# Optimization experiments

Hardware: AMD Instinct MI355X
Metric: run time of the kernel (lower is better)

Reference implementation:

```python
import jax, jax.numpy as jnp
import numpy as np

N_CELLS = 8192
IN_DIM = 512
HID_DIM = 1024
OUT_DIM = 512
ENG_DIM = 128  # hardcoded MLP width in BenchMind
N_FACTIONS = 8
SYNC = 0.15
DEBATE = 0.15


def setup_inputs() -> dict:
    key = jax.random.key(0)
    ks = iter(jax.random.split(key, 40))

    def rn(shape, s=1.0):
        return jax.random.normal(next(ks), shape, dtype=jnp.float32) * s

    def lin(out_d, in_d):
        s = 1.0 / np.sqrt(in_d)
        return rn((out_d, in_d), s), rn((out_d,), s)

    a_W1, a_b1 = lin(ENG_DIM, IN_DIM + HID_DIM)
    a_W2, a_b2 = lin(OUT_DIM, ENG_DIM)
    g_W1, g_b1 = lin(ENG_DIM, IN_DIM + HID_DIM)
    g_W2, g_b2 = lin(OUT_DIM, ENG_DIM)
    gru_Wih, gru_bih = lin(3 * HID_DIM, OUT_DIM + 1)
    gru_Whh, gru_bhh = lin(3 * HID_DIM, HID_DIM)
    proj_W, proj_b = lin(HID_DIM, 2 * HID_DIM)
    head_W, head_b = lin(IN_DIM, OUT_DIM)

    psi = rn((N_CELLS, HID_DIM), 0.1)
    psi = psi / (jnp.linalg.norm(psi, axis=-1, keepdims=True) + 1e-8)
    rho_diag = psi ** 2
    rho_offdiag = rn((N_CELLS, HID_DIM), 0.1)
    hiddens = rn((N_CELLS, HID_DIM), 0.1)
    noise_diag = rn((N_CELLS, HID_DIM))
    noise_off = rn((N_CELLS, HID_DIM))
    x = rn((1, IN_DIM))
    gamma = jnp.float32(0.1)

    return dict(x=x, rho_diag=rho_diag, rho_offdiag=rho_offdiag, hiddens=hiddens,
                gamma=gamma, proj_W=proj_W, proj_b=proj_b,
                a_W1=a_W1, a_b1=a_b1, a_W2=a_W2, a_b2=a_b2,
                g_W1=g_W1, g_b1=g_b1, g_W2=g_W2, g_b2=g_b2,
                gru_Wih=gru_Wih, gru_bih=gru_bih, gru_Whh=gru_Whh, gru_bhh=gru_bhh,
                head_W=head_W, head_b=head_b,
                noise_diag=noise_diag, noise_off=noise_off, step=10)


def _process(x, rho_diag, rho_offdiag, hiddens, gamma, proj_W, proj_b,
             a_W1, a_b1, a_W2, a_b2, g_W1, g_b1, g_W2, g_b2,
             gru_Wih, gru_bih, gru_Whh, gru_bhh, head_W, head_b,
             noise_diag, noise_off, step):
    n = hiddens.shape[0]
    # --- decohere() --- (gamma used via .item() in torch -> non-differentiable)
    g = jax.lax.stop_gradient(jax.nn.sigmoid(gamma))
    rho_off = rho_offdiag * (1.0 - g)
    rho_d = jax.nn.softmax(rho_diag + noise_diag * g * 0.1, axis=-1)
    feat = jnp.concatenate([rho_d, jnp.abs(rho_off)], axis=-1)        # [N, 2H]
    inj = feat @ proj_W.T + proj_b                                     # [N, H]
    h = hiddens + jax.lax.stop_gradient(inj) * 0.1

    # --- batched BenchMind over all cells (torch loops cells one-by-one) ---
    xb = jnp.broadcast_to(x, (n, x.shape[-1]))
    comb = jnp.concatenate([xb, h], axis=-1)                           # [N, I+H]
    a = jax.nn.relu(comb @ a_W1.T + a_b1) @ a_W2.T + a_b2              # [N, O]
    gg = jax.nn.relu(comb @ g_W1.T + g_b1) @ g_W2.T + g_b2             # [N, O]
    out = a - gg
    tension = jnp.mean(out ** 2, axis=-1, keepdims=True)               # [N, 1]

    # GRUCell (torch gate order: r, z, n); inputs are detached in torch
    mem_in = jax.lax.stop_gradient(jnp.concatenate([out, tension], axis=-1))
    gi = mem_in @ gru_Wih.T + gru_bih                                  # [N, 3H]
    gh = h @ gru_Whh.T + gru_bhh                                       # [N, 3H]
    i_r, i_z, i_n = jnp.split(gi, 3, axis=-1)
    h_r, h_z, h_n = jnp.split(gh, 3, axis=-1)
    r = jax.nn.sigmoid(i_r + h_r)
    z = jax.nn.sigmoid(i_z + h_z)
    nn_ = jnp.tanh(i_n + r * h_n)
    new_h = jax.lax.stop_gradient((1.0 - z) * nn_ + z * h)             # .detach() in torch

    # --- faction_sync_debate ---
    nf = min(N_FACTIONS, n // 2)
    fs = n // nf
    hb = new_h[: nf * fs].reshape(nf, fs, -1)
    hb = (1.0 - SYNC) * hb + SYNC * hb.mean(axis=1, keepdims=True)
    if step > 5:
        glob = hb.mean(axis=1).mean(axis=0)                            # [H]
        dc = max(1, fs // 4)
        hb = hb.at[:, :dc].set((1.0 - DEBATE) * hb[:, :dc] + DEBATE * glob)
    new_h = hb.reshape(nf * fs, -1)

    # --- tension-weighted mixture (weights built from .item()s -> no grad) ---
    w = jax.nn.softmax(jax.lax.stop_gradient(tension[:, 0]))           # [N]
    combined = (w[:, None] * out).sum(axis=0, keepdims=True)           # [1, O]
    pred = combined @ head_W.T + head_b                                # [1, I]
    return pred, new_h


def reference(x, rho_diag, rho_offdiag, hiddens, gamma, proj_W, proj_b,
              a_W1, a_b1, a_W2, a_b2, g_W1, g_b1, g_W2, g_b2,
              gru_Wih, gru_bih, gru_Whh, gru_bhh, head_W, head_b,
              noise_diag, noise_off, step):
    return _process(x, rho_diag, rho_offdiag, hiddens, gamma, proj_W, proj_b,
                    a_W1, a_b1, a_W2, a_b2, g_W1, g_b1, g_W2, g_b2,
                    gru_Wih, gru_bih, gru_Whh, gru_bhh, head_W, head_b,
                    noise_diag, noise_off, step)
```

## Files before the change

kernel.cpp:

```cpp
#include <hip/hip_runtime.h>
#include <math.h>

#define NC 8192
#define ID 512
#define HD 1024
#define OD 512
#define ED 128
#define NF 8
#define FS (NC/NF)
#define DC (FS/4)

typedef __bf16 bf16x8 __attribute__((ext_vector_type(8)));
typedef float  f32x4  __attribute__((ext_vector_type(4)));

__device__ __forceinline__ float sigmf(float x){ return 1.0f/(1.0f+__expf(-x)); }

__device__ __forceinline__ unsigned short f2bf(float f){
  union { float f; unsigned u; } v; v.f = f;
  unsigned r = v.u + 0x7FFFu + ((v.u >> 16) & 1u);
  return (unsigned short)(r >> 16);
}
__device__ __forceinline__ float bf2f(unsigned short b){
  union { unsigned u; float f; } v; v.u = ((unsigned)b) << 16;
  return v.f;
}
__device__ __forceinline__ void gload16(const void* g, void* l){
  __builtin_amdgcn_global_load_lds(
      (const __attribute__((address_space(1))) unsigned int*)g,
      (__attribute__((address_space(3))) unsigned int*)l, 16, 0, 0);
}

__global__ __launch_bounds__(256) void k_conv(
    const float* __restrict__ src, unsigned short* __restrict__ dst,
    int rows, int cols, int sld, int sofs, int dld, float scale)
{
  int i = blockIdx.x*256 + threadIdx.x;
  int total = rows*cols/4;
  if (i >= total) return;
  int r = (i*4)/cols, c = (i*4)%cols;
  const float* s = src + (size_t)r*sld + sofs + c;
  unsigned long long pack = 0;
  for (int q=0;q<4;q++)
    pack |= (unsigned long long)f2bf(s[q]*scale) << (16*q);
  *reinterpret_cast<unsigned long long*>(&dst[(size_t)r*dld + c]) = pack;
}

__global__ __launch_bounds__(256) void k_feat(
    const float* __restrict__ rho_diag, const float* __restrict__ noise_diag,
    const float* __restrict__ rho_off,  const float* __restrict__ gamma,
    unsigned short* __restrict__ featb)
{
  int row = blockIdx.x;
  int t = threadIdx.x;
  float g = 1.0f/(1.0f+__expf(-gamma[0]));
  const float* rd = rho_diag  + (size_t)row*HD;
  const float* nd = noise_diag+ (size_t)row*HD;
  const float* ro = rho_off   + (size_t)row*HD;
  unsigned short* f0 = featb + (size_t)row*(2*HD);

  float v[4];
  float mx = -1e30f;
  for (int i=0;i<4;i++){ int j=t+i*256; v[i] = rd[j] + nd[j]*g*0.1f; mx = fmaxf(mx, v[i]); }
  __shared__ float red[256];
  red[t]=mx; __syncthreads();
  for(int s=128;s>0;s>>=1){ if(t<s) red[t]=fmaxf(red[t],red[t+s]); __syncthreads(); }
  mx = red[0]; __syncthreads();
  float sm=0.0f;
  for(int i=0;i<4;i++){ v[i]=__expf(v[i]-mx); sm+=v[i]; }
  red[t]=sm; __syncthreads();
  for(int s=128;s>0;s>>=1){ if(t<s) red[t]+=red[t+s]; __syncthreads(); }
  float inv = 1.0f/red[0];
  float om_g = 1.0f - g;
  for(int i=0;i<4;i++){
    int j=t+i*256;
    f0[j]     = f2bf(v[i]*inv);
    f0[HD+j]  = f2bf(fabsf(ro[j])*om_g);
  }
}

template<int MODE>
__global__ __launch_bounds__(256) void k_mgemm(
    const unsigned short* __restrict__ A,
    const unsigned short* __restrict__ W,
    int K, int N,
    float* __restrict__ Cf, unsigned short* __restrict__ Cb, int ldc,
    const float* __restrict__ e0, const float* __restrict__ e1,
    const float* __restrict__ e2)
{
  __shared__ __attribute__((aligned(16))) unsigned short Asb[128*32];
  __shared__ __attribute__((aligned(16))) unsigned short Bsb[128*32];
  const int t = threadIdx.x;
  const int lane = t & 63, wid = t >> 6;
  const int wr = wid >> 1, wc = wid & 1;
  const int m0 = blockIdx.y * 128, n0 = blockIdx.x * 128;

  const int srow = lane >> 2;
  const int skch = (lane & 3) * 8;
  const int fr = lane & 15, fk = (lane >> 4) * 8;

  f32x4 acc[4][4] = {};
  for (int k0 = 0; k0 < K; k0 += 32) {
    for (int q = 0; q < 2; ++q) {
      int r = wid*32 + q*16 + srow;
      gload16(A + (size_t)(m0 + r)*K + k0 + skch, &Asb[(wid*32 + q*16)*32]);
      gload16(W + (size_t)(n0 + r)*K + k0 + skch, &Bsb[(wid*32 + q*16)*32]);
    }
    __syncthreads();
    bf16x8 af[4], bfr[4];
    for (int i = 0; i < 4; ++i)
      af[i]  = *reinterpret_cast<const bf16x8*>(&Asb[(wr*64 + i*16 + fr)*32 + fk]);
    for (int j = 0; j < 4; ++j)
      bfr[j] = *reinterpret_cast<const bf16x8*>(&Bsb[(wc*64 + j*16 + fr)*32 + fk]);
    for (int i = 0; i < 4; ++i)
      for (int j = 0; j < 4; ++j)
        acc[i][j] = __builtin_amdgcn_mfma_f32_16x16x32_bf16(af[i], bfr[j], acc[i][j], 0, 0, 0);
    __syncthreads();
  }
  const int cr = (lane >> 4) * 4;
  const int cc = lane & 15;
  for (int i = 0; i < 4; ++i){
    for (int j = 0; j < 4; ++j){
      for (int r = 0; r < 4; ++r){
        int m = m0 + wr*64 + i*16 + cr + r;
        int n = n0 + wc*64 + j*16 + cc;
        float v = acc[i][j][r];
        if (MODE == 0)      v = e0[(size_t)m*N + n] + 0.1f*(v + e1[n]);
        else if (MODE == 1) v = fmaxf(v + e0[n], 0.0f);
        else if (MODE == 2) v = v + e0[n];
        else if (MODE == 4) v = v + e0[n] + e1[m]*e2[n];
        size_t o = (size_t)m*ldc + n;
        if (MODE == 0 || MODE == 2) Cf[o] = v;
        Cb[o] = f2bf(v);
      }
    }
  }
}

__global__ __launch_bounds__(128) void k_xpart(
    const float* __restrict__ x,
    const float* __restrict__ aW1, const float* __restrict__ ab1,
    const float* __restrict__ gW1, const float* __restrict__ gb1,
    const float* __restrict__ Wih,
    const float* __restrict__ ab2, const float* __restrict__ gb2,
    float* __restrict__ xcat, float* __restrict__ wlast, float* __restrict__ b2diff)
{
  int t = threadIdx.x;
  if (blockIdx.x == 2){
    for (int n=t; n<3*HD; n+=128) wlast[n] = Wih[(size_t)n*(OD+1) + OD];
    for (int n=t; n<OD;   n+=128) b2diff[n] = ab2[n] - gb2[n];
    return;
  }
  const float* W = blockIdx.x ? gW1 : aW1;
  const float* b = blockIdx.x ? gb1 : ab1;
  float s = b[t];
  const float* wr = W + (size_t)t*(ID+HD);
  for (int k=0;k<ID;k++) s += x[k]*wr[k];
  xcat[blockIdx.x*ED + t] = s;
}

__global__ __launch_bounds__(256) void k_tension(
    const float* __restrict__ outp, float* __restrict__ tens)
{
  int m = blockIdx.x, t = threadIdx.x;
  float s = 0.0f;
  for (int j=t;j<OD;j+=256){ float v = outp[(size_t)m*OD + j]; s += v*v; }
  __shared__ float red[256];
  red[t]=s; __syncthreads();
  for(int k=128;k>0;k>>=1){ if(t<k) red[t]+=red[t+k]; __syncthreads(); }
  if (t==0) tens[m] = red[0] * (1.0f/OD);
}

__global__ __launch_bounds__(256) void k_gru_elem(
    const unsigned short* __restrict__ gi, const unsigned short* __restrict__ gh,
    const float* __restrict__ h, const float* __restrict__ bhh,
    float* __restrict__ newh)
{
  size_t idx = (size_t)blockIdx.x*256 + threadIdx.x;
  int n = (int)(idx & (HD-1));
  size_t m = idx >> 10;
  size_t b = m*(3*HD) + n;
  float i_r = bf2f(gi[b]), i_z = bf2f(gi[b+HD]), i_n = bf2f(gi[b+2*HD]);
  float h_r = bf2f(gh[b]), h_z = bf2f(gh[b+HD]), h_n = bf2f(gh[b+2*HD]);
  float r  = sigmf(i_r + h_r + bhh[n]);
  float z  = sigmf(i_z + h_z + bhh[HD+n]);
  float nn = tanhf(i_n + r*(h_n + bhh[2*HD+n]));
  newh[idx] = (1.0f-z)*nn + z*h[idx];
}

__global__ __launch_bounds__(256) void k_fmean(
    const float* __restrict__ newh, float* __restrict__ fmean)
{
  int f = blockIdx.x;
  int j = blockIdx.y*256 + threadIdx.x;
  const float* base = newh + (size_t)f*FS*HD + j;
  float s = 0.0f;
  for (int c=0;c<FS;c++) s += base[(size_t)c*HD];
  fmean[f*HD + j] = s * (1.0f/FS);
}

__global__ __launch_bounds__(256) void k_sync(
    float* __restrict__ newh, const float* __restrict__ fmean,
    const int* __restrict__ step)
{
  size_t idx = (size_t)blockIdx.x*256 + threadIdx.x;
  int cell = (int)(idx / HD);
  int j    = (int)(idx % HD);
  int f = cell / FS, c = cell % FS;
  float v = newh[idx];
  v = 0.85f*v + 0.15f*fmean[f*HD + j];
  if (step[0] > 5 && c < DC){
    float glob = 0.0f;
    for (int ff=0; ff<NF; ff++) glob += fmean[ff*HD + j];
    glob *= (1.0f/NF);
    v = 0.85f*v + 0.15f*glob;
  }
  newh[idx] = v;
}

__global__ __launch_bounds__(1024) void k_wstats(
    const float* __restrict__ tens, float* __restrict__ stats)
{
  int t = threadIdx.x;
  float mx = -1e30f;
  for (int i=t;i<NC;i+=1024) mx = fmaxf(mx, tens[i]);
  __shared__ float red[1024];
  red[t]=mx; __syncthreads();
  for(int s=512;s>0;s>>=1){ if(t<s) red[t]=fmaxf(red[t],red[t+s]); __syncthreads(); }
  mx = red[0]; __syncthreads();
  float sm=0.0f;
  for (int i=t;i<NC;i+=1024) sm += __expf(tens[i]-mx);
  red[t]=sm; __syncthreads();
  for(int s=512;s>0;s>>=1){ if(t<s) red[t]+=red[t+s]; __syncthreads(); }
  if (t==0){ stats[0]=mx; stats[1]=red[0]; }
}

__global__ __launch_bounds__(256) void k_wnorm(
    const float* __restrict__ tens, const float* __restrict__ stats,
    float* __restrict__ w)
{
  int m = blockIdx.x*256 + threadIdx.x;
  w[m] = __expf(tens[m]-stats[0]) * (1.0f/stats[1]);
}

__global__ __launch_bounds__(256) void k_combined(
    const float* __restrict__ outp, const float* __restrict__ w,
    float* __restrict__ comb)
{
  int n = blockIdx.x, t = threadIdx.x;
  float s = 0.0f;
  for (int m=t; m<NC; m+=256) s += w[m]*outp[(size_t)m*OD + n];
  __shared__ float red[256];
  red[t]=s; __syncthreads();
  for (int sx=128;sx>0;sx>>=1){ if(t<sx) red[t]+=red[t+sx]; __syncthreads(); }
  if (t==0) comb[n] = red[0];
}

__global__ __launch_bounds__(128) void k_pred(
    const float* __restrict__ comb, const float* __restrict__ headW,
    const float* __restrict__ headb, float* __restrict__ pred)
{
  int i = blockIdx.x, t = threadIdx.x;
  float s = 0.0f;
  const float* wr = headW + (size_t)i*OD;
  for (int k=t;k<OD;k+=128) s += comb[k]*wr[k];
  __shared__ float red[128];
  red[t]=s; __syncthreads();
  for (int sx=64;sx>0;sx>>=1){ if(t<sx) red[t]+=red[t+sx]; __syncthreads(); }
  if (t==0) pred[i] = red[0] + headb[i];
}

extern "C" void kernel_launch(void* const* d_in, const int* in_sizes, int n_in,
                              void* d_out, int out_size, void* d_ws, size_t ws_size,
                              hipStream_t stream)
{
  const float* x        = (const float*)d_in[0];
  const float* rho_diag = (const float*)d_in[1];
  const float* rho_off  = (const float*)d_in[2];
  const float* hiddens  = (const float*)d_in[3];
  const float* gamma    = (const float*)d_in[4];
  const float* proj_W   = (const float*)d_in[5];
  const float* proj_b   = (const float*)d_in[6];
  const float* a_W1     = (const float*)d_in[7];
  const float* a_b1     = (const float*)d_in[8];
  const float* a_W2     = (const float*)d_in[9];
  const float* a_b2     = (const float*)d_in[10];
  const float* g_W1     = (const float*)d_in[11];
  const float* g_b1     = (const float*)d_in[12];
  const float* g_W2     = (const float*)d_in[13];
  const float* g_b2     = (const float*)d_in[14];
  const float* gru_Wih  = (const float*)d_in[15];
  const float* gru_bih  = (const float*)d_in[16];
  const float* gru_Whh  = (const float*)d_in[17];
  const float* gru_bhh  = (const float*)d_in[18];
  const float* head_W   = (const float*)d_in[19];
  const float* head_b   = (const float*)d_in[20];
  const float* noise_d  = (const float*)d_in[21];
  const int*   step     = (const int*)d_in[23];

  float* pred = (float*)d_out;
  float* newh = (float*)d_out + ID;

  char* ws = (char*)d_ws;
  const size_t MB = 1024*1024;
  unsigned short* gi_b   = (unsigned short*)(ws + 0);
  unsigned short* featb  = (unsigned short*)(ws + 0);
  unsigned short* gh_b   = (unsigned short*)(ws + 48*MB);
  float*          h_f    = (float*)(ws + 96*MB);
  unsigned short* h_b    = (unsigned short*)(ws + 128*MB);
  float*          outp_f = (float*)(ws + 144*MB);
  unsigned short* outp_b = (unsigned short*)(ws + 160*MB);
  unsigned short* eag    = (unsigned short*)(ws + 168*MB);
  unsigned short* wProj  = (unsigned short*)(ws + 172*MB);
  unsigned short* wWhh   = (unsigned short*)(ws + 176*MB);
  unsigned short* wWih   = (unsigned short*)(ws + 182*MB);
  unsigned short* wEng   = (unsigned short*)(ws + 185*MB);
  unsigned short* wW2    = (unsigned short*)(ws + 185*MB + 512*1024);
  char* sm = ws + 186*MB;
  float* tens   = (float*)(sm + 0);
  float* xcat   = (float*)(sm + 64*1024);
  float* wlast  = (float*)(sm + 128*1024);
  float* b2diff = (float*)(sm + 160*1024);
  float* fmean  = (float*)(sm + 192*1024);
  float* stats  = (float*)(sm + 256*1024);
  float* wts    = (float*)(sm + 320*1024);
  float* comb   = (float*)(sm + 384*1024);

  dim3 blk(256);
  #define CONVGRID(n) dim3(((n)/4 + 255)/256)

  k_conv<<<CONVGRID(1024*2048), blk, 0, stream>>>(proj_W,  wProj, 1024, 2048, 2048, 0, 2048, 1.0f);
  k_conv<<<CONVGRID(3072*1024), blk, 0, stream>>>(gru_Whh, wWhh,  3072, 1024, 1024, 0, 1024, 1.0f);
  k_conv<<<CONVGRID(3072*512),  blk, 0, stream>>>(gru_Wih, wWih,  3072, 512,  513,  0, 512,  1.0f);
  k_conv<<<CONVGRID(128*1024),  blk, 0, stream>>>(a_W1, wEng,            128, 1024, ID+HD, ID, 1024, 1.0f);
  k_conv<<<CONVGRID(128*1024),  blk, 0, stream>>>(g_W1, wEng + 128*1024, 128, 1024, ID+HD, ID, 1024, 1.0f);
  k_conv<<<CONVGRID(512*128),   blk, 0, stream>>>(a_W2, wW2,       512, 128, 128, 0, 256,  1.0f);
  k_conv<<<CONVGRID(512*128),   blk, 0, stream>>>(g_W2, wW2 + 128, 512, 128, 128, 0, 256, -1.0f);

  k_feat<<<dim3(NC), blk, 0, stream>>>(rho_diag, noise_d, rho_off, gamma, featb);
  k_xpart<<<dim3(3), dim3(128), 0, stream>>>(x, a_W1, a_b1, g_W1, g_b1, gru_Wih,
                                             a_b2, g_b2, xcat, wlast, b2diff);

  k_mgemm<0><<<dim3(HD/128, NC/128), blk, 0, stream>>>(
      featb, wProj, 2*HD, HD, h_f, h_b, HD, hiddens, proj_b, nullptr);
  k_mgemm<1><<<dim3(256/128, NC/128), blk, 0, stream>>>(
      h_b, wEng, HD, 256, nullptr, eag, 256, xcat, nullptr, nullptr);
  k_mgemm<2><<<dim3(OD/128, NC/128), blk, 0, stream>>>(
      eag, wW2, 256, OD, outp_f, outp_b, OD, b2diff, nullptr, nullptr);
  k_tension<<<dim3(NC), blk, 0, stream>>>(outp_f, tens);
  k_mgemm<4><<<dim3(3*HD/128, NC/128), blk, 0, stream>>>(
      outp_b, wWih, OD, 3*HD, nullptr, gi_b, 3*HD, gru_bih, tens, wlast);
  k_mgemm<3><<<dim3(3*HD/128, NC/128), blk, 0, stream>>>(
      h_b, wWhh, HD, 3*HD, nullptr, gh_b, 3*HD, nullptr, nullptr, nullptr);
  k_gru_elem<<<dim3((NC*HD)/256), blk, 0, stream>>>(gi_b, gh_b, h_f, gru_bhh, newh);
  k_fmean<<<dim3(NF, HD/256), blk, 0, stream>>>(newh, fmean);
  k_sync<<<dim3((NC*HD)/256), blk, 0, stream>>>(newh, fmean, step);
  k_wstats<<<dim3(1), dim3(1024), 0, stream>>>(tens, stats);
  k_wnorm<<<dim3(NC/256), blk, 0, stream>>>(tens, stats, wts);
  k_combined<<<dim3(OD), blk, 0, stream>>>(outp_f, wts, comb);
  k_pred<<<dim3(ID), dim3(128), 0, stream>>>(comb, head_W, head_b, pred);
}
```

Before: 623.6 us.

## Fuse GRU input and hidden GEMMs with gate epilogue into one kernel

Concatenates the engine output and hidden state into one bf16 activation buffer and packs Wih/Whh into one weight matrix. A single GEMM kernel then computes the r, z and n gate pre-activations in registers and applies the GRU update in its epilogue. This removes the separate gi/gh bf16 intermediates and the elementwise pass. It also adds a grouped block-index swizzle to the GEMMs and splits the weighted-mixture reduction into a two-stage partial sum. The fused kernel uses 64x64 tiles with one wave loading each operand tile, which may lower MFMA efficiency compared with the previous 128x128 tiles.

```diff
diff --git a/kernel.cpp b/kernel.cpp
--- a/kernel.cpp
+++ b/kernel.cpp
@@ -43,6 +43,25 @@
   for (int q=0;q<4;q++)
     pack |= (unsigned long long)f2bf(s[q]*scale) << (16*q);
   *reinterpret_cast<unsigned long long*>(&dst[(size_t)r*dld + c]) = pack;
+}
+
+__global__ __launch_bounds__(256) void k_convgru(
+    const float* __restrict__ Wih, const float* __restrict__ Whh,
+    unsigned short* __restrict__ dst)
+{
+  int i = blockIdx.x*256 + threadIdx.x;
+  const int total = 3*1024*1536/4;
+  if (i >= total) return;
+  int row = (i*4)/1536, c = (i*4)%1536;
+  unsigned long long pack = 0;
+  if (c < 512){
+    const float* s = Wih + (size_t)row*(OD+1) + c;
+    for (int q=0;q<4;q++) pack |= (unsigned long long)f2bf(s[q]) << (16*q);
+  } else {
+    const float* s = Whh + (size_t)row*HD + (c-512);
+    for (int q=0;q<4;q++) pack |= (unsigned long long)f2bf(s[q]) << (16*q);
+  }
+  *reinterpret_cast<unsigned long long*>(&dst[(size_t)row*1536 + c]) = pack;
 }
 
 __global__ __launch_bounds__(256) void k_feat(
@@ -80,19 +99,23 @@
 
 template<int MODE>
 __global__ __launch_bounds__(256) void k_mgemm(
-    const unsigned short* __restrict__ A,
+    const unsigned short* __restrict__ A, int lda,
     const unsigned short* __restrict__ W,
     int K, int N,
-    float* __restrict__ Cf, unsigned short* __restrict__ Cb, int ldc,
-    const float* __restrict__ e0, const float* __restrict__ e1,
-    const float* __restrict__ e2)
+    float* __restrict__ Cf, int ldcf,
+    unsigned short* __restrict__ Cb, int ldcb,
+    const float* __restrict__ e0, const float* __restrict__ e1)
 {
   __shared__ __attribute__((aligned(16))) unsigned short Asb[128*32];
   __shared__ __attribute__((aligned(16))) unsigned short Bsb[128*32];
   const int t = threadIdx.x;
   const int lane = t & 63, wid = t >> 6;
   const int wr = wid >> 1, wc = wid & 1;
-  const int m0 = blockIdx.y * 128, n0 = blockIdx.x * 128;
+
+  const int nwg = gridDim.x*gridDim.y;
+  const int bid = blockIdx.y*gridDim.x + blockIdx.x;
+  const int swz = (bid & 7)*(nwg >> 3) + (bid >> 3);
+  const int m0 = (swz / gridDim.x) * 128, n0 = (swz % gridDim.x) * 128;
 
   const int srow = lane >> 2;
   const int skch = (lane & 3) * 8;
@@ -102,8 +125,8 @@
   for (int k0 = 0; k0 < K; k0 += 32) {
     for (int q = 0; q < 2; ++q) {
       int r = wid*32 + q*16 + srow;
-      gload16(A + (size_t)(m0 + r)*K + k0 + skch, &Asb[(wid*32 + q*16)*32]);
-      gload16(W + (size_t)(n0 + r)*K + k0 + skch, &Bsb[(wid*32 + q*16)*32]);
+      gload16(A + (size_t)(m0 + r)*lda + k0 + skch, &Asb[(wid*32 + q*16)*32]);
+      gload16(W + (size_t)(n0 + r)*K   + k0 + skch, &Bsb[(wid*32 + q*16)*32]);
     }
     __syncthreads();
     bf16x8 af[4], bfr[4];
@@ -127,10 +150,93 @@
         if (MODE == 0)      v = e0[(size_t)m*N + n] + 0.1f*(v + e1[n]);
         else if (MODE == 1) v = fmaxf(v + e0[n], 0.0f);
         else if (MODE == 2) v = v + e0[n];
-        else if (MODE == 4) v = v + e0[n] + e1[m]*e2[n];
-        size_t o = (size_t)m*ldc + n;
-        if (MODE == 0 || MODE == 2) Cf[o] = v;
-        Cb[o] = f2bf(v);
+        if (MODE == 2) Cf[(size_t)m*ldcf + n] = v;
+        Cb[(size_t)m*ldcb + n] = f2bf(v);
+      }
+    }
+  }
+}
+
+__global__ __launch_bounds__(256) void k_gru_mega(
+    const unsigned short* __restrict__ Acat,
+    const unsigned short* __restrict__ Wg,
+    const float* __restrict__ bih, const float* __restrict__ bhh,
+    const float* __restrict__ tens, const float* __restrict__ wlast,
+    float* __restrict__ newh)
+{
+  __shared__ __attribute__((aligned(16))) unsigned short As[64*32];
+  __shared__ __attribute__((aligned(16))) unsigned short Rs[64*32];
+  __shared__ __attribute__((aligned(16))) unsigned short Zs[64*32];
+  __shared__ __attribute__((aligned(16))) unsigned short Ns[64*32];
+  const int t = threadIdx.x;
+  const int lane = t & 63, wid = t >> 6;
+  const int wr = wid >> 1, wc = wid & 1;
+
+  const int nwg = gridDim.x*gridDim.y;
+  const int bid = blockIdx.y*gridDim.x + blockIdx.x;
+  const int swz = (bid & 7)*(nwg >> 3) + (bid >> 3);
+  const int m0 = (swz >> 4) * 64, n0 = (swz & 15) * 64;
+
+  const int srow = lane >> 2;
+  const int skch = (lane & 3) * 8;
+  const int fr = lane & 15, fk = (lane >> 4) * 8;
+
+  const unsigned short* sbase;
+  unsigned short* lbase;
+  if      (wid == 0){ sbase = Acat + (size_t)m0*1536;              lbase = As; }
+  else if (wid == 1){ sbase = Wg   + (size_t)n0*1536;              lbase = Rs; }
+  else if (wid == 2){ sbase = Wg + (size_t)(HD + n0)*1536;         lbase = Zs; }
+  else              { sbase = Wg + (size_t)(2*HD + n0)*1536;       lbase = Ns; }
+
+  f32x4 acc_r[2][2] = {}, acc_z[2][2] = {}, acc_na[2][2] = {}, acc_nb[2][2] = {};
+
+  for (int k0 = 0; k0 < 1536; k0 += 32) {
+    for (int q = 0; q < 4; ++q)
+      gload16(sbase + (size_t)(q*16 + srow)*1536 + k0 + skch, &lbase[(q*16)*32]);
+    __syncthreads();
+    bf16x8 af[2], br[2], bz[2], bn[2];
+    for (int i = 0; i < 2; ++i)
+      af[i] = *reinterpret_cast<const bf16x8*>(&As[(wr*32 + i*16 + fr)*32 + fk]);
+    for (int j = 0; j < 2; ++j){
+      br[j] = *reinterpret_cast<const bf16x8*>(&Rs[(wc*32 + j*16 + fr)*32 + fk]);
+      bz[j] = *reinterpret_cast<const bf16x8*>(&Zs[(wc*32 + j*16 + fr)*32 + fk]);
+      bn[j] = *reinterpret_cast<const bf16x8*>(&Ns[(wc*32 + j*16 + fr)*32 + fk]);
+    }
+    if (k0 < 512){
+      for (int i = 0; i < 2; ++i)
+        for (int j = 0; j < 2; ++j){
+          acc_r [i][j] = __builtin_amdgcn_mfma_f32_16x16x32_bf16(af[i], br[j], acc_r [i][j], 0,0,0);
+          acc_z [i][j] = __builtin_amdgcn_mfma_f32_16x16x32_bf16(af[i], bz[j], acc_z [i][j], 0,0,0);
+          acc_na[i][j] = __builtin_amdgcn_mfma_f32_16x16x32_bf16(af[i], bn[j], acc_na[i][j], 0,0,0);
+        }
+    } else {
+      for (int i = 0; i < 2; ++i)
+        for (int j = 0; j < 2; ++j){
+          acc_r [i][j] = __builtin_amdgcn_mfma_f32_16x16x32_bf16(af[i], br[j], acc_r [i][j], 0,0,0);
+          acc_z [i][j] = __builtin_amdgcn_mfma_f32_16x16x32_bf16(af[i], bz[j], acc_z [i][j], 0,0,0);
+          acc_nb[i][j] = __builtin_amdgcn_mfma_f32_16x16x32_bf16(af[i], bn[j], acc_nb[i][j], 0,0,0);
+        }
+    }
+    __syncthreads();
+  }
+
+  const int cr = (lane >> 4) * 4;
+  const int cc = lane & 15;
+  for (int i = 0; i < 2; ++i){
+    for (int r = 0; r < 4; ++r){
+      int m = m0 + wr*32 + i*16 + cr + r;
+      float tm = tens[m];
+      for (int j = 0; j < 2; ++j){
+        int n = n0 + wc*32 + j*16 + cc;
+        float sr  = acc_r [i][j][r] + bih[n]      + tm*wlast[n]      + bhh[n];
+        float sz  = acc_z [i][j][r] + bih[HD+n]   + tm*wlast[HD+n]   + bhh[HD+n];
+        float sni = acc_na[i][j][r] + bih[2*HD+n] + tm*wlast[2*HD+n];
+        float snh = acc_nb[i][j][r] + bhh[2*HD+n];
+        float rg = sigmf(sr);
+        float zg = sigmf(sz);
+        float nn = tanhf(sni + rg*snh);
+        float hv = bf2f(Acat[(size_t)m*1536 + 512 + n]);
+        newh[(size_t)m*HD + n] = (1.0f - zg)*nn + zg*hv;
       }
     }
   }
@@ -168,23 +274,6 @@
   red[t]=s; __syncthreads();
   for(int k=128;k>0;k>>=1){ if(t<k) red[t]+=red[t+k]; __syncthreads(); }
   if (t==0) tens[m] = red[0] * (1.0f/OD);
-}
-
-__global__ __launch_bounds__(256) void k_gru_elem(
-    const unsigned short* __restrict__ gi, const unsigned short* __restrict__ gh,
-    const float* __restrict__ h, const float* __restrict__ bhh,
-    float* __restrict__ newh)
-{
-  size_t idx = (size_t)blockIdx.x*256 + threadIdx.x;
-  int n = (int)(idx & (HD-1));
-  size_t m = idx >> 10;
-  size_t b = m*(3*HD) + n;
-  float i_r = bf2f(gi[b]), i_z = bf2f(gi[b+HD]), i_n = bf2f(gi[b+2*HD]);
-  float h_r = bf2f(gh[b]), h_z = bf2f(gh[b+HD]), h_n = bf2f(gh[b+2*HD]);
-  float r  = sigmf(i_r + h_r + bhh[n]);
-  float z  = sigmf(i_z + h_z + bhh[HD+n]);
-  float nn = tanhf(i_n + r*(h_n + bhh[2*HD+n]));
-  newh[idx] = (1.0f-z)*nn + z*h[idx];
 }
 
 __global__ __launch_bounds__(256) void k_fmean(
@@ -242,17 +331,30 @@
   w[m] = __expf(tens[m]-stats[0]) * (1.0f/stats[1]);
 }
 
-__global__ __launch_bounds__(256) void k_combined(
+__global__ __launch_bounds__(256) void k_comb1(
     const float* __restrict__ outp, const float* __restrict__ w,
-    float* __restrict__ comb)
-{
-  int n = blockIdx.x, t = threadIdx.x;
+    float* __restrict__ partial)
+{
+  int b = blockIdx.x, t = threadIdx.x;
+  float a0 = 0.0f, a1 = 0.0f;
+  for (int m = 0; m < 128; ++m){
+    int row = b*128 + m;
+    float wm = w[row];
+    const float* r = outp + (size_t)row*OD;
+    a0 += wm * r[t];
+    a1 += wm * r[t+256];
+  }
+  partial[(size_t)b*OD + t]       = a0;
+  partial[(size_t)b*OD + t + 256] = a1;
+}
+
+__global__ __launch_bounds__(256) void k_comb2(
+    const float* __restrict__ partial, float* __restrict__ comb)
+{
+  int n = blockIdx.x*256 + threadIdx.x;
   float s = 0.0f;
-  for (int m=t; m<NC; m+=256) s += w[m]*outp[(size_t)m*OD + n];
-  __shared__ float red[256];
-  red[t]=s; __syncthreads();
-  for (int sx=128;sx>0;sx>>=1){ if(t<sx) red[t]+=red[t+sx]; __syncthreads(); }
-  if (t==0) comb[n] = red[0];
+  for (int b = 0; b < 64; ++b) s += partial[(size_t)b*OD + n];
+  comb[n] = s;
 }
 
 __global__ __launch_bounds__(128) void k_pred(
@@ -302,60 +404,53 @@
 
   char* ws = (char*)d_ws;
   const size_t MB = 1024*1024;
-  unsigned short* gi_b   = (unsigned short*)(ws + 0);
-  unsigned short* featb  = (unsigned short*)(ws + 0);
-  unsigned short* gh_b   = (unsigned short*)(ws + 48*MB);
-  float*          h_f    = (float*)(ws + 96*MB);
-  unsigned short* h_b    = (unsigned short*)(ws + 128*MB);
-  float*          outp_f = (float*)(ws + 144*MB);
-  unsigned short* outp_b = (unsigned short*)(ws + 160*MB);
-  unsigned short* eag    = (unsigned short*)(ws + 168*MB);
-  unsigned short* wProj  = (unsigned short*)(ws + 172*MB);
-  unsigned short* wWhh   = (unsigned short*)(ws + 176*MB);
-  unsigned short* wWih   = (unsigned short*)(ws + 182*MB);
-  unsigned short* wEng   = (unsigned short*)(ws + 185*MB);
-  unsigned short* wW2    = (unsigned short*)(ws + 185*MB + 512*1024);
-  char* sm = ws + 186*MB;
-  float* tens   = (float*)(sm + 0);
-  float* xcat   = (float*)(sm + 64*1024);
-  float* wlast  = (float*)(sm + 128*1024);
-  float* b2diff = (float*)(sm + 160*1024);
-  float* fmean  = (float*)(sm + 192*1024);
-  float* stats  = (float*)(sm + 256*1024);
-  float* wts    = (float*)(sm + 320*1024);
-  float* comb   = (float*)(sm + 384*1024);
+  unsigned short* Acat   = (unsigned short*)(ws + 0);
+  unsigned short* featb  = (unsigned short*)(ws + 24*MB);
+  float*          outp_f = (float*)(ws + 56*MB);
+  unsigned short* eag    = (unsigned short*)(ws + 72*MB);
+  unsigned short* wProj  = (unsigned short*)(ws + 76*MB);
+  unsigned short* wGru   = (unsigned short*)(ws + 80*MB);
+  unsigned short* wEng   = (unsigned short*)(ws + 89*MB);
+  unsigned short* wW2    = (unsigned short*)(ws + 89*MB + 512*1024);
+  char* sm = ws + 90*MB;
+  float* tens    = (float*)(sm + 0);
+  float* xcat    = (float*)(sm + 64*1024);
+  float* wlast   = (float*)(sm + 128*1024);
+  float* b2diff  = (float*)(sm + 160*1024);
+  float* fmean   = (float*)(sm + 192*1024);
+  float* stats   = (float*)(sm + 256*1024);
+  float* wts     = (float*)(sm + 320*1024);
+  float* partial = (float*)(sm + 384*1024);
+  float* comb    = (float*)(sm + 576*1024);
 
   dim3 blk(256);
   #define CONVGRID(n) dim3(((n)/4 + 255)/256)
 
-  k_conv<<<CONVGRID(1024*2048), blk, 0, stream>>>(proj_W,  wProj, 1024, 2048, 2048, 0, 2048, 1.0f);
-  k_conv<<<CONVGRID(3072*1024), blk, 0, stream>>>(gru_Whh, wWhh,  3072, 1024, 1024, 0, 1024, 1.0f);
-  k_conv<<<CONVGRID(3072*512),  blk, 0, stream>>>(gru_Wih, wWih,  3072, 512,  513,  0, 512,  1.0f);
-  k_conv<<<CONVGRID(128*1024),  blk, 0, stream>>>(a_W1, wEng,            128, 1024, ID+HD, ID, 1024, 1.0f);
-  k_conv<<<CONVGRID(128*1024),  blk, 0, stream>>>(g_W1, wEng + 128*1024, 128, 1024, ID+HD, ID, 1024, 1.0f);
-  k_conv<<<CONVGRID(512*128),   blk, 0, stream>>>(a_W2, wW2,       512, 128, 128, 0, 256,  1.0f);
-  k_conv<<<CONVGRID(512*128),   blk, 0, stream>>>(g_W2, wW2 + 128, 512, 128, 128, 0, 256, -1.0f);
+  k_conv<<<CONVGRID(1024*2048), blk, 0, stream>>>(proj_W, wProj, 1024, 2048, 2048, 0, 2048, 1.0f);
+  k_convgru<<<dim3(3*1024*1536/4/256), blk, 0, stream>>>(gru_Wih, gru_Whh, wGru);
+  k_conv<<<CONVGRID(128*1024), blk, 0, stream>>>(a_W1, wEng,            128, 1024, ID+HD, ID, 1024, 1.0f);
+  k_conv<<<CONVGRID(128*1024), blk, 0, stream>>>(g_W1, wEng + 128*1024, 128, 1024, ID+HD, ID, 1024, 1.0f);
+  k_conv<<<CONVGRID(512*128),  blk, 0, stream>>>(a_W2, wW2,       512, 128, 128, 0, 256,  1.0f);
+  k_conv<<<CONVGRID(512*128),  blk, 0, stream>>>(g_W2, wW2 + 128, 512, 128, 128, 0, 256, -1.0f);
 
   k_feat<<<dim3(NC), blk, 0, stream>>>(rho_diag, noise_d, rho_off, gamma, featb);
   k_xpart<<<dim3(3), dim3(128), 0, stream>>>(x, a_W1, a_b1, g_W1, g_b1, gru_Wih,
                                              a_b2, g_b2, xcat, wlast, b2diff);
 
   k_mgemm<0><<<dim3(HD/128, NC/128), blk, 0, stream>>>(
-      featb, wProj, 2*HD, HD, h_f, h_b, HD, hiddens, proj_b, nullptr);
+      featb, 2*HD, wProj, 2*HD, HD, nullptr, 0, Acat + 512, 1536, hiddens, proj_b);
   k_mgemm<1><<<dim3(256/128, NC/128), blk, 0, stream>>>(
-      h_b, wEng, HD, 256, nullptr, eag, 256, xcat, nullptr, nullptr);
+      Acat + 512, 1536, wEng, HD, 256, nullptr, 0, eag, 256, xcat, nullptr);
   k_mgemm<2><<<dim3(OD/128, NC/128), blk, 0, stream>>>(
-      eag, wW2, 256, OD, outp_f, outp_b, OD, b2diff, nullptr, nullptr);
+      eag, 256, wW2, 256, OD, outp_f, OD, Acat, 1536, b2diff, nullptr);
   k_tension<<<dim3(NC), blk, 0, stream>>>(outp_f, tens);
-  k_mgemm<4><<<dim3(3*HD/128, NC/128), blk, 0, stream>>>(
-      outp_b, wWih, OD, 3*HD, nullptr, gi_b, 3*HD, gru_bih, tens, wlast);
-  k_mgemm<3><<<dim3(3*HD/128, NC/128), blk, 0, stream>>>(
-      h_b, wWhh, HD, 3*HD, nullptr, gh_b, 3*HD, nullptr, nullptr, nullptr);
-  k_gru_elem<<<dim3((NC*HD)/256), blk, 0, stream>>>(gi_b, gh_b, h_f, gru_bhh, newh);
+  k_gru_mega<<<dim3(HD/64, NC/64), blk, 0, stream>>>(
+      Acat, wGru, gru_bih, gru_bhh, tens, wlast, newh);
   k_fmean<<<dim3(NF, HD/256), blk, 0, stream>>>(newh, fmean);
   k_sync<<<dim3((NC*HD)/256), blk, 0, stream>>>(newh, fmean, step);
   k_wstats<<<dim3(1), dim3(1024), 0, stream>>>(tens, stats);
   k_wnorm<<<dim3(NC/256), blk, 0, stream>>>(tens, stats, wts);
-  k_combined<<<dim3(OD), blk, 0, stream>>>(outp_f, wts, comb);
+  k_comb1<<<dim3(64), blk, 0, stream>>>(outp_f, wts, partial);
+  k_comb2<<<dim3(2), blk, 0, stream>>>(partial, comb);
   k_pred<<<dim3(ID), dim3(128), 0, stream>>>(comb, head_W, head_b, pred);
 }
```

Measured after the change: 602.8 us. 3.3% less time.
